# Kernel optimization log

Hardware: AMD Instinct MI355X
Metric: run time of the kernel (lower is better)

## Reference

```python
import jax, jax.numpy as jnp
import numpy as np
from jax import lax

N_QUBITS = 8
N_BLOCKS = 5

_H = jnp.array([[1.0, 1.0], [1.0, -1.0]], dtype=jnp.complex64) / np.sqrt(2.0).astype(np.float32)
# torchquantum PauliY.diagonalizing_gates = [Z, S, H] applied in order -> matrix H @ S @ Z = H @ diag(1, -1j)
_YROT = _H @ jnp.diag(jnp.array([1.0, -1j], dtype=jnp.complex64))


def apply_gate(st, U, wires):
    # st: [N, 2, 2, ..., 2] (n_qubits trailing axes); U: [2^k, 2^k]
    k = len(wires)
    axes = [w + 1 for w in wires]
    s = jnp.moveaxis(st, axes, list(range(1, k + 1)))
    shp = s.shape
    s = s.reshape(shp[0], 2 ** k, -1)
    s = jnp.einsum('ij,bjr->bir', U, s)
    return jnp.moveaxis(s.reshape(shp), list(range(1, k + 1)), axes)


def u3_mat(th, ph, lam):
    c = jnp.cos(0.5 * th).astype(jnp.complex64)
    s = jnp.sin(0.5 * th).astype(jnp.complex64)
    el = jnp.exp(1j * lam)
    ep = jnp.exp(1j * ph)
    return jnp.stack([jnp.stack([c, -el * s]), jnp.stack([ep * s, ep * el * c])])


def cu3_mat(th, ph, lam):
    M = jnp.eye(4, dtype=jnp.complex64)
    return M.at[2:, 2:].set(u3_mat(th, ph, lam))


def z_expvals(st):
    # <Z_w> for every wire from marginal probabilities
    n = st.ndim - 1
    mag = st.real ** 2 + st.imag ** 2
    outs = []
    for w in range(n):
        axes = tuple(a for a in range(1, n + 1) if a != w + 1)
        p = mag.sum(axes)  # [N, 2]
        outs.append(p[:, 0] - p[:, 1])
    return jnp.stack(outs, axis=1)


def quantum_conv(x, conv_w, conv_b, u3_params, cu3_params, fc_w, fc_b):
    n = N_QUBITS
    B, C, H, W = x.shape
    y = lax.conv_general_dilated(x, conv_w, (1, 1), 'SAME',
                                 dimension_numbers=('NCHW', 'OIHW', 'NCHW'))
    y = y + conv_b[None, :, None, None]
    ang = y.transpose(0, 2, 3, 1).reshape(-1, n)  # [B*H*W, n_qubits]
    Npx = ang.shape[0]
    # RY(theta)|0> encoding: product state of [cos(t/2), sin(t/2)] per wire
    c = jnp.cos(0.5 * ang)
    s = jnp.sin(0.5 * ang)
    st = jnp.stack([c[:, 0], s[:, 0]], axis=1).astype(jnp.complex64)
    for w in range(1, n):
        q = jnp.stack([c[:, w], s[:, w]], axis=1).astype(jnp.complex64)
        st = (st[:, :, None] * q[:, None, :]).reshape(Npx, -1)
    st = st.reshape((Npx,) + (2,) * n)
    # U3CU3Layer0: per block, U3 on each wire then circular CU3 ring
    for b in range(N_BLOCKS):
        for w in range(n):
            st = apply_gate(st, u3_mat(u3_params[b, w, 0], u3_params[b, w, 1], u3_params[b, w, 2]), [w])
        for w in range(n):
            st = apply_gate(st, cu3_mat(cu3_params[b, w, 0], cu3_params[b, w, 1], cu3_params[b, w, 2]), [w, (w + 1) % n])
    # MeasureAll(Z), then MeasureAll(X) and MeasureAll(Y) which MUTATE the device
    # state with their diagonalizing gates (torchquantum semantics)
    mz = z_expvals(st)
    for w in range(n):
        st = apply_gate(st, _H, [w])
    mx = z_expvals(st)
    for w in range(n):
        st = apply_gate(st, _YROT, [w])
    my = z_expvals(st)
    meas = jnp.concatenate([mz, mx, my], axis=1)  # [B*H*W, 3*n]
    out = meas @ fc_w.T + fc_b
    return out.reshape(B, H, W, -1).transpose(0, 3, 1, 2)


def setup_inputs() -> dict:
    key = jax.random.key(0)
    ks = jax.random.split(key, 7)
    n, cin, cout = N_QUBITS, 16, 32
    x = jax.random.normal(ks[0], (4, cin, 64, 64), dtype=jnp.float32)
    conv_w = jax.random.normal(ks[1], (n, cin, 3, 3), dtype=jnp.float32) / np.sqrt(cin * 9)
    conv_b = jax.random.normal(ks[2], (n,), dtype=jnp.float32) * 0.01
    u3_params = jax.random.uniform(ks[3], (N_BLOCKS, n, 3), dtype=jnp.float32, minval=-np.pi, maxval=np.pi)
    cu3_params = jax.random.uniform(ks[4], (N_BLOCKS, n, 3), dtype=jnp.float32, minval=-np.pi, maxval=np.pi)
    fc_w = jax.random.normal(ks[5], (cout, 3 * n), dtype=jnp.float32) / np.sqrt(3 * n)
    fc_b = jax.random.normal(ks[6], (cout,), dtype=jnp.float32) * 0.01
    return {'x': x, 'conv_w': conv_w, 'conv_b': conv_b, 'u3_params': u3_params,
            'cu3_params': cu3_params, 'fc_w': fc_w, 'fc_b': fc_b}


def reference(x, conv_w, conv_b, u3_params, cu3_params, fc_w, fc_b):
    return quantum_conv(x, conv_w, conv_b, u3_params, cu3_params, fc_w, fc_b)
```

## Files before the change

### kernel.cpp

```cpp
#include <hip/hip_runtime.h>

typedef float v2f __attribute__((ext_vector_type(2)));

template<int C>
__device__ __forceinline__ float dppmov(float x) {
  return __int_as_float(__builtin_amdgcn_update_dpp(0, __float_as_int(x), C, 0xF, 0xF, true));
}
__device__ __forceinline__ float bperm(float x, int a) {
  return __int_as_float(__builtin_amdgcn_ds_bpermute(a, __float_as_int(x)));
}
template<int M>
__device__ __forceinline__ float bfly(float x) {
  if constexpr (M == 1)      return dppmov<0xB1>(x);
  else if constexpr (M == 2) return dppmov<0x4E>(x);
  else if constexpr (M == 3) return dppmov<0x1B>(x);
  else if constexpr (M == 8) return dppmov<0x128>(x);
  else                       return dppmov<0x1B>(dppmov<0x141>(x));
}
template<int M>
__device__ __forceinline__ v2f bfly2(v2f v) {
  v2f o; o.x = bfly<M>(v.x); o.y = bfly<M>(v.y); return o;
}
__device__ __forceinline__ v2f sp(float s) { v2f v; v.x = s; v.y = s; return v; }
__device__ __forceinline__ v2f vfma(v2f a, v2f b, v2f c) {
  return __builtin_elementwise_fma(a, b, c);
}

template<int M, int CM>
__device__ __forceinline__ void crossG(v2f Sr[16], v2f Si[16],
    const float* g, int lane) {
  const bool hi = (lane & M) != 0;
  const bool ct = (lane & CM) != 0;
  float f0r = hi ? g[6]  : g[0],  f0i = hi ? g[7]  : g[1];
  float g0r = hi ? g[4]  : g[2],  g0i = hi ? g[5]  : g[3];
  float f1r = hi ? g[14] : g[8],  f1i = hi ? g[15] : g[9];
  float g1r = hi ? g[12] : g[10], g1i = hi ? g[13] : g[11];
  float fr = ct ? f1r : f0r, fi = ct ? f1i : f0i;
  float gr = ct ? g1r : g0r, gi = ct ? g1i : g0i;
  v2f vfr = sp(fr), vfi = sp(fi), vgr = sp(gr), vgi = sp(gi);
  v2f vfiN = sp(-fi), vgiN = sp(-gi);
#pragma unroll
  for (int r = 0; r < 16; ++r) {
    v2f pR = bfly2<M>(Sr[r]);
    v2f pI = bfly2<M>(Si[r]);
    v2f nR = vfma(vgiN, pI, vfma(vgr, pR, vfma(vfiN, Si[r], vfr * Sr[r])));
    v2f nI = vfma(vgi,  pR, vfma(vgr, pI, vfma(vfi,  Sr[r], vfr * Si[r])));
    Sr[r] = nR; Si[r] = nI;
  }
}

__device__ __forceinline__ void mixP(v2f& x0r, v2f& x0i, v2f& x1r, v2f& x1i,
    float m0r, float m0i, float m1r, float m1i,
    float m2r, float m2i, float m3r, float m3i) {
  v2f n0r = vfma(sp(-m1i), x1i, vfma(sp(m1r), x1r, vfma(sp(-m0i), x0i, sp(m0r) * x0r)));
  v2f n0i = vfma(sp( m1i), x1r, vfma(sp(m1r), x1i, vfma(sp( m0i), x0r, sp(m0r) * x0i)));
  v2f n1r = vfma(sp(-m3i), x1i, vfma(sp(m3r), x1r, vfma(sp(-m2i), x0i, sp(m2r) * x0r)));
  v2f n1i = vfma(sp( m3i), x1r, vfma(sp(m3r), x1i, vfma(sp( m2i), x0r, sp(m2r) * x0i)));
  x0r = n0r; x0i = n0i; x1r = n1r; x1i = n1i;
}

__device__ __forceinline__ void f4N(v2f Sr[16], v2f Si[16],
    const float* g, int lane) {
  const bool ct = (lane & 1) != 0;
  float m[8];
#pragma unroll
  for (int jj = 0; jj < 8; ++jj) m[jj] = ct ? g[8 + jj] : g[jj];
#pragma unroll
  for (int r = 0; r < 8; ++r)
    mixP(Sr[r], Si[r], Sr[r + 8], Si[r + 8],
         m[0], m[1], m[2], m[3], m[4], m[5], m[6], m[7]);
}
__device__ __forceinline__ void f5N(v2f Sr[16], v2f Si[16], const float* g) {
#pragma unroll
  for (int r = 0; r < 4; ++r)
    mixP(Sr[r], Si[r], Sr[r + 4], Si[r + 4],
         g[0], g[1], g[2], g[3], g[4], g[5], g[6], g[7]);
#pragma unroll
  for (int r = 8; r < 12; ++r)
    mixP(Sr[r], Si[r], Sr[r + 4], Si[r + 4],
         g[8], g[9], g[10], g[11], g[12], g[13], g[14], g[15]);
}
__device__ __forceinline__ void f67N(v2f Sr[16], v2f Si[16], const float* T) {
#pragma unroll
  for (int qd = 0; qd < 4; ++qd) {
    const int B = qd * 4;
    const float* M = T + (qd & 1) * 32;
    v2f ar0 = Sr[B+0], ai0 = Si[B+0], ar1 = Sr[B+1], ai1 = Si[B+1];
    v2f ar2 = Sr[B+2], ai2 = Si[B+2], ar3 = Sr[B+3], ai3 = Si[B+3];
#pragma unroll
    for (int rp = 0; rp < 4; ++rp) {
      const float* Mr = M + rp * 8;
      v2f nR = sp(Mr[0]) * ar0;
      nR = vfma(sp(-Mr[1]), ai0, nR);
      nR = vfma(sp( Mr[2]), ar1, nR);
      nR = vfma(sp(-Mr[3]), ai1, nR);
      nR = vfma(sp( Mr[4]), ar2, nR);
      nR = vfma(sp(-Mr[5]), ai2, nR);
      nR = vfma(sp( Mr[6]), ar3, nR);
      nR = vfma(sp(-Mr[7]), ai3, nR);
      v2f nI = sp(Mr[1]) * ar0;
      nI = vfma(sp(Mr[0]), ai0, nI);
      nI = vfma(sp(Mr[3]), ar1, nI);
      nI = vfma(sp(Mr[2]), ai1, nI);
      nI = vfma(sp(Mr[5]), ar2, nI);
      nI = vfma(sp(Mr[4]), ai2, nI);
      nI = vfma(sp(Mr[7]), ar3, nI);
      nI = vfma(sp(Mr[6]), ai3, nI);
      Sr[B + rp] = nR; Si[B + rp] = nI;
    }
  }
}
__device__ __forceinline__ void f8pN(v2f Sr[16], v2f Si[16],
    const float* g, int lane) {
  const bool hi = (lane & 8) != 0;
  float fr[2], fi[2], gr[2], gi[2];
  fr[0] = hi ? g[6]  : g[0];  fi[0] = hi ? g[7]  : g[1];
  gr[0] = hi ? g[4]  : g[2];  gi[0] = hi ? g[5]  : g[3];
  fr[1] = hi ? g[14] : g[8];  fi[1] = hi ? g[15] : g[9];
  gr[1] = hi ? g[12] : g[10]; gi[1] = hi ? g[13] : g[11];
#pragma unroll
  for (int r = 0; r < 16; ++r) {
    const int m = r & 1;
    v2f pR = bfly2<8>(Sr[r]);
    v2f pI = bfly2<8>(Si[r]);
    v2f nR = vfma(sp(-gi[m]), pI, vfma(sp(gr[m]), pR, vfma(sp(-fi[m]), Si[r], sp(fr[m]) * Sr[r])));
    v2f nI = vfma(sp( gi[m]), pR, vfma(sp(gr[m]), pI, vfma(sp( fi[m]), Sr[r], sp(fr[m]) * Si[r])));
    Sr[r] = nR; Si[r] = nI;
  }
}
__device__ __forceinline__ void f8N(v2f Sr[16], v2f Si[16],
    const float* g, int lane) {
  const bool hi = (lane & 8) != 0;
  const float fr = hi ? g[6] : g[0], fi = hi ? g[7] : g[1];
  const float gr = hi ? g[4] : g[2], gi = hi ? g[5] : g[3];
#pragma unroll
  for (int r = 1; r < 16; r += 2) {
    v2f pR = bfly2<8>(Sr[r]);
    v2f pI = bfly2<8>(Si[r]);
    v2f nR = vfma(sp(-gi), pI, vfma(sp(gr), pR, vfma(sp(-fi), Si[r], sp(fr) * Sr[r])));
    v2f nI = vfma(sp( gi), pR, vfma(sp(gr), pI, vfma(sp( fi), Sr[r], sp(fr) * Si[r])));
    Sr[r] = nR; Si[r] = nI;
  }
}

template<int M>
__device__ __forceinline__ void crossO(const v2f Sr[16], const v2f Si[16],
                                       v2f& re, v2f& im) {
  v2f r = sp(0.0f), i = sp(0.0f);
#pragma unroll
  for (int k = 0; k < 16; ++k) {
    v2f pr = bfly2<M>(Sr[k]);
    v2f pi = bfly2<M>(Si[k]);
    r = vfma(Sr[k], pr, r);
    r = vfma(Si[k], pi, r);
    i = vfma(Si[k], pr, i);
    i = vfma(-Sr[k], pi, i);
  }
  re = r; im = i;
}

__device__ __forceinline__ void mm2(const float* A, const float* B, float* D) {
  D[0] = A[0]*B[0] - A[1]*B[1] + A[2]*B[4] - A[3]*B[5];
  D[1] = A[0]*B[1] + A[1]*B[0] + A[2]*B[5] + A[3]*B[4];
  D[2] = A[0]*B[2] - A[1]*B[3] + A[2]*B[6] - A[3]*B[7];
  D[3] = A[0]*B[3] + A[1]*B[2] + A[2]*B[7] + A[3]*B[6];
  D[4] = A[4]*B[0] - A[5]*B[1] + A[6]*B[4] - A[7]*B[5];
  D[5] = A[4]*B[1] + A[5]*B[0] + A[6]*B[5] + A[7]*B[4];
  D[6] = A[4]*B[2] - A[5]*B[3] + A[6]*B[6] - A[7]*B[7];
  D[7] = A[4]*B[3] + A[5]*B[2] + A[6]*B[7] + A[7]*B[6];
}
__device__ __forceinline__ void u3fill(const float* src, float* o) {
  float th = src[0], ph = src[1], lam = src[2];
  float c = cosf(0.5f * th), s = sinf(0.5f * th);
  float cl = cosf(lam), sl = sinf(lam);
  float cp = cosf(ph), spv = sinf(ph);
  float cpl = cosf(ph + lam), spl = sinf(ph + lam);
  o[0] = c;        o[1] = 0.0f;
  o[2] = -cl * s;  o[3] = -sl * s;
  o[4] = cp * s;   o[5] = spv * s;
  o[6] = cpl * c;  o[7] = spl * c;
}

__global__ __launch_bounds__(256) void qconv_kernel(
    const float* __restrict__ x, const float* __restrict__ cw,
    const float* __restrict__ cb, const float* __restrict__ u3p,
    const float* __restrict__ cu3p, const float* __restrict__ fcw,
    const float* __restrict__ fcb, float* __restrict__ out) {
  __shared__ float Us[40][8];
  __shared__ float Cs[40][8];
  __shared__ float Gs[640];
  __shared__ float FCWs[32 * 29];
  __shared__ float F67t[320];

  {
    const int t = threadIdx.x;
    if (t < 40) u3fill(u3p + t * 3, Us[t]);
    if (t >= 64 && t < 104) u3fill(cu3p + (t - 64) * 3, Cs[t - 64]);
    for (int i = t; i < 32 * 29; i += 256) {
      int ch = i / 29, u = i - ch * 29;
      float v = 0.0f;
      if (u < 24) {
        float sc = (u >= 8 && (u & 7) >= 4) ? 2.0f : 1.0f;
        v = fcw[ch * 24 + u] * sc;
      }
      FCWs[i] = v;
    }
    __syncthreads();
    if (t == 0) {
#pragma unroll
      for (int j = 0; j < 8; ++j) Gs[j] = Us[0][j];
    } else if (t < 36) {
      int j = t - 1, b = j / 7, k = j % 7;
      float* dst = Gs + 8 + b * 112 + k * 16;
      const float* U = Us[b * 8 + k + 1];
      const float* C = Cs[b * 8 + k];
#pragma unroll
      for (int u = 0; u < 8; ++u) dst[u] = U[u];
      mm2(C, U, dst + 8);
    } else if (t < 40) {
      int b = t - 36;
      float* dst = Gs + 568 + b * 16;
      const float* U = Us[(b + 1) * 8];
      const float* C = Cs[b * 8 + 7];
#pragma unroll
      for (int u = 0; u < 8; ++u) dst[u] = U[u];
      mm2(U, C, dst + 8);
    } else if (t == 40) {
#pragma unroll
      for (int j = 0; j < 8; ++j) Gs[632 + j] = Cs[39][j];
    }
    __syncthreads();
    if (t >= 64 && t < 104) {
      int u = t - 64;
      int b = u >> 3, idx = u & 7;
      int ct = idx >> 2, rp = idx & 3;
      const float* M6 = Gs + 8 + b * 112 + 80 + ct * 8;
      int b1p = rp >> 1, b0p = rp & 1;
      const float* M7 = Gs + 8 + b * 112 + 96 + b1p * 8;
      float* dst = F67t + b * 64 + ct * 32 + rp * 8;
#pragma unroll
      for (int c = 0; c < 4; ++c) {
        int b1 = c >> 1, b0 = c & 1;
        float a_r = M6[(b1p * 2 + b1) * 2], a_i = M6[(b1p * 2 + b1) * 2 + 1];
        float b_r = M7[(b0p * 2 + b0) * 2], b_i = M7[(b0p * 2 + b0) * 2 + 1];
        dst[c * 2]     = a_r * b_r - a_i * b_i;
        dst[c * 2 + 1] = a_r * b_i + a_i * b_r;
      }
    }
    __syncthreads();
  }

  const int lane = threadIdx.x & 63;
  const int wid = __builtin_amdgcn_readfirstlane(
      (int)((blockIdx.x * blockDim.x + threadIdx.x) >> 6));
  const int p0 = wid * 8;
  const int q = lane & 15;

  float ang;
  {
    const int px = lane >> 3;
    const int oc = lane & 7;
    const int p  = p0 + px;
    const int b  = p >> 12;
    const int hh = (p >> 6) & 63;
    const int wim = p & 63;
    float acc = cb[oc];
#pragma unroll 4
    for (int ic = 0; ic < 16; ++ic) {
      const float* wp = cw + (oc * 16 + ic) * 9;
      const float* xp = x + (b * 16 + ic) * 4096;
#pragma unroll
      for (int kh = 0; kh < 3; ++kh) {
        int ih = hh + kh - 1;
        bool rok = (unsigned)ih < 64u;
        int ihc = rok ? ih : 0;
#pragma unroll
        for (int kw = 0; kw < 3; ++kw) {
          int iw = wim + kw - 1;
          bool ok = rok && ((unsigned)iw < 64u);
          int iwc = ((unsigned)iw < 64u) ? iw : 0;
          float xv = xp[ihc * 64 + iwc];
          acc = fmaf(ok ? xv : 0.0f, wp[kh * 3 + kw], acc);
        }
      }
    }
    ang = acc;
  }

  v2f Sr[16], Si[16];
  {
    const int gb = (lane & 48) << 2;
    float aA[8], aB[8];
#pragma unroll
    for (int w = 0; w < 8; ++w) {
      aA[w] = bperm(ang, gb + (w << 2));
      aB[w] = bperm(ang, gb + ((8 + w) << 2));
    }
    float cA[8], sA[8], cB[8], sB[8];
#pragma unroll
    for (int w = 0; w < 8; ++w) {
      __sincosf(0.5f * aA[w], &sA[w], &cA[w]);
      __sincosf(0.5f * aB[w], &sB[w], &cB[w]);
    }
    v2f c0; c0.x = cA[0]; c0.y = cB[0];
    v2f s0; s0.x = sA[0]; s0.y = sB[0];
    v2f c0r = vfma(sp(Gs[2]), s0, sp(Gs[0]) * c0);
    v2f c0i = vfma(sp(Gs[3]), s0, sp(Gs[1]) * c0);
    v2f s0r = vfma(sp(Gs[6]), s0, sp(Gs[4]) * c0);
    v2f s0i = vfma(sp(Gs[7]), s0, sp(Gs[5]) * c0);
    const bool w0 = (q & 8) != 0;
    v2f selR = w0 ? s0r : c0r;
    v2f selI = w0 ? s0i : c0i;
    float fA = ((q & 4) ? sA[1] : cA[1]) * ((q & 2) ? sA[2] : cA[2])
             * ((q & 1) ? sA[3] : cA[3]);
    float fB = ((q & 4) ? sB[1] : cB[1]) * ((q & 2) ? sB[2] : cB[2])
             * ((q & 1) ? sB[3] : cB[3]);
    v2f uu[4], vv[4];
    uu[0].x = cA[6]*cA[7]; uu[1].x = cA[6]*sA[7];
    uu[2].x = sA[6]*cA[7]; uu[3].x = sA[6]*sA[7];
    uu[0].y = cB[6]*cB[7]; uu[1].y = cB[6]*sB[7];
    uu[2].y = sB[6]*cB[7]; uu[3].y = sB[6]*sB[7];
    float vA0 = fA * cA[4], vA1 = fA * sA[4];
    float vB0 = fB * cB[4], vB1 = fB * sB[4];
    vv[0].x = vA0*cA[5]; vv[1].x = vA0*sA[5];
    vv[2].x = vA1*cA[5]; vv[3].x = vA1*sA[5];
    vv[0].y = vB0*cB[5]; vv[1].y = vB0*sB[5];
    vv[2].y = vB1*cB[5]; vv[3].y = vB1*sB[5];
#pragma unroll
    for (int r = 0; r < 16; ++r) {
      v2f base = vv[r >> 2] * uu[r & 3];
      Sr[r] = selR * base;
      Si[r] = selI * base;
    }
  }

  for (int b = 0; b < 5; ++b) {
    const float* base = Gs + 8 + b * 112;
    crossG<4, 8>(Sr, Si, base + 0, lane);
    crossG<2, 4>(Sr, Si, base + 16, lane);
    crossG<1, 2>(Sr, Si, base + 32, lane);
    f4N(Sr, Si, base + 48, lane);
    f5N(Sr, Si, base + 64);
    f67N(Sr, Si, F67t + b * 64);
    if (b < 4) f8pN(Sr, Si, Gs + 568 + b * 16, lane);
  }
  f8N(Sr, Si, Gs + 632, lane);

  float sg[4];
  sg[0] = (q & 8) ? -1.0f : 1.0f;
  sg[1] = (q & 4) ? -1.0f : 1.0f;
  sg[2] = (q & 2) ? -1.0f : 1.0f;
  sg[3] = (q & 1) ? -1.0f : 1.0f;

  v2f PT[24];
  {
    v2f re0, im0, re1, im1, re2, im2, re3, im3;
    crossO<8>(Sr, Si, re0, im0);
    crossO<4>(Sr, Si, re1, im1);
    crossO<2>(Sr, Si, re2, im2);
    crossO<1>(Sr, Si, re3, im3);
    PT[8]  = re0; PT[9]  = re1; PT[10] = re2; PT[11] = re3;
    PT[16] = sp(sg[0]) * im0; PT[17] = sp(sg[1]) * im1;
    PT[18] = sp(sg[2]) * im2; PT[19] = sp(sg[3]) * im3;

    v2f P[16];
#pragma unroll
    for (int r = 0; r < 16; ++r) P[r] = vfma(Si[r], Si[r], Sr[r] * Sr[r]);
    v2f t01[8];
#pragma unroll
    for (int k = 0; k < 8; ++k) t01[k] = P[2*k] + P[2*k+1];
    v2f q0 = t01[0] + t01[1], q1 = t01[2] + t01[3];
    v2f q2 = t01[4] + t01[5], q3 = t01[6] + t01[7];
    v2f h0 = q0 + q1, h1 = q2 + q3;
    v2f p  = h0 + h1;
    PT[4] = h0 - h1;
    PT[5] = (q0 - q1) + (q2 - q3);
    PT[6] = (t01[0]-t01[1]) + (t01[2]-t01[3])
          + (t01[4]-t01[5]) + (t01[6]-t01[7]);
    PT[7] = (P[0]-P[1]) + (P[2]-P[3]) + (P[4]-P[5]) + (P[6]-P[7])
          + (P[8]-P[9]) + (P[10]-P[11]) + (P[12]-P[13]) + (P[14]-P[15]);
    PT[0] = sp(sg[0]) * p; PT[1] = sp(sg[1]) * p;
    PT[2] = sp(sg[2]) * p; PT[3] = sp(sg[3]) * p;

    v2f re, im;
    re = sp(0.0f); im = sp(0.0f);
#pragma unroll
    for (int r = 0; r < 8; ++r) {
      re = vfma(Sr[r], Sr[r+8], re); re = vfma(Si[r], Si[r+8], re);
      im = vfma(Si[r], Sr[r+8], im); im = vfma(-Sr[r], Si[r+8], im);
    }
    PT[12] = re; PT[20] = im;
    re = sp(0.0f); im = sp(0.0f);
#pragma unroll
    for (int t = 0; t < 8; ++t) {
      const int lo = (t & 3) + (t >> 2) * 8;
      re = vfma(Sr[lo], Sr[lo+4], re); re = vfma(Si[lo], Si[lo+4], re);
      im = vfma(Si[lo], Sr[lo+4], im); im = vfma(-Sr[lo], Si[lo+4], im);
    }
    PT[13] = re; PT[21] = im;
    re = sp(0.0f); im = sp(0.0f);
#pragma unroll
    for (int t = 0; t < 8; ++t) {
      const int lo = (t & 1) + (t >> 1) * 4;
      re = vfma(Sr[lo], Sr[lo+2], re); re = vfma(Si[lo], Si[lo+2], re);
      im = vfma(Si[lo], Sr[lo+2], im); im = vfma(-Sr[lo], Si[lo+2], im);
    }
    PT[14] = re; PT[22] = im;
    re = sp(0.0f); im = sp(0.0f);
#pragma unroll
    for (int t = 0; t < 8; ++t) {
      const int lo = 2 * t;
      re = vfma(Sr[lo], Sr[lo+1], re); re = vfma(Si[lo], Si[lo+1], re);
      im = vfma(Si[lo], Sr[lo+1], im); im = vfma(-Sr[lo], Si[lo+1], im);
    }
    PT[15] = re; PT[23] = im;
  }

  const int j = q & 7;
  const bool isB = (q & 8) != 0;
  float mm[24];
#pragma unroll
  for (int t = 0; t < 24; ++t) {
    v2f v = PT[t] + bfly2<8>(PT[t]);
    float s = isB ? v.y : v.x;
    s += bfly<1>(s);
    s += bfly<2>(s);
    s += bfly<4>(s);
    mm[t] = s;
  }

  const int g = lane >> 4;
  const int p = p0 + 2 * g + (isB ? 1 : 0);
  const int ob = (p >> 12) * 131072 + (p & 4095);
#pragma unroll
  for (int k = 0; k < 4; ++k) {
    const int ch = 4 * j + k;
    const float* wr = FCWs + ch * 29;
    float acc = fcb[ch];
#pragma unroll
    for (int u = 0; u < 24; ++u) acc = fmaf(mm[u], wr[u], acc);
    out[ob + ch * 4096] = acc;
  }
}

extern "C" void kernel_launch(void* const* d_in, const int* in_sizes, int n_in,
                              void* d_out, int out_size, void* d_ws, size_t ws_size,
                              hipStream_t stream) {
  const float* x      = (const float*)d_in[0];
  const float* conv_w = (const float*)d_in[1];
  const float* conv_b = (const float*)d_in[2];
  const float* u3p    = (const float*)d_in[3];
  const float* cu3p   = (const float*)d_in[4];
  const float* fcw    = (const float*)d_in[5];
  const float* fcb    = (const float*)d_in[6];
  float* out = (float*)d_out;

  qconv_kernel<<<512, 256, 0, stream>>>(x, conv_w, conv_b, u3p, cu3p,
                                        fcw, fcb, out);
}
```

Baseline: 108.1 us.

## Prefetch gate coefficients from LDS into registers ahead of each gate stage

The gate-application loop now loads each stage's coefficients from shared memory into register arrays with 128-bit vector loads, one stage ahead of use. This is meant to hide LDS latency behind the butterfly arithmetic. It also switches the U3 trig setup to fast __sincosf and adds a min-blocks-per-CU launch bound of 2. The extra register arrays (about 96 floats) and the occupancy hint may raise register pressure or cause spills.

```diff
diff --git a/kernel.cpp b/kernel.cpp
--- a/kernel.cpp
+++ b/kernel.cpp
@@ -1,6 +1,7 @@
 #include <hip/hip_runtime.h>
 
 typedef float v2f __attribute__((ext_vector_type(2)));
+typedef float v4f __attribute__((ext_vector_type(4)));
 
 template<int C>
 __device__ __forceinline__ float dppmov(float x) {
@@ -24,6 +25,25 @@
 __device__ __forceinline__ v2f sp(float s) { v2f v; v.x = s; v.y = s; return v; }
 __device__ __forceinline__ v2f vfma(v2f a, v2f b, v2f c) {
   return __builtin_elementwise_fma(a, b, c);
+}
+
+__device__ __forceinline__ void ld16(float* d, const float* s) {
+  const v4f* p = (const v4f*)s;
+  v4f a = p[0], b = p[1], c = p[2], e = p[3];
+  d[0]=a.x; d[1]=a.y; d[2]=a.z; d[3]=a.w;
+  d[4]=b.x; d[5]=b.y; d[6]=b.z; d[7]=b.w;
+  d[8]=c.x; d[9]=c.y; d[10]=c.z; d[11]=c.w;
+  d[12]=e.x; d[13]=e.y; d[14]=e.z; d[15]=e.w;
+}
+__device__ __forceinline__ void ld8(float* d, const float* s) {
+  const v4f* p = (const v4f*)s;
+  v4f a = p[0], b = p[1];
+  d[0]=a.x; d[1]=a.y; d[2]=a.z; d[3]=a.w;
+  d[4]=b.x; d[5]=b.y; d[6]=b.z; d[7]=b.w;
+}
+__device__ __forceinline__ void ld64(float* d, const float* s) {
+#pragma unroll
+  for (int k = 0; k < 4; ++k) ld16(d + k * 16, s + k * 16);
 }
 
 template<int M, int CM>
@@ -171,26 +191,27 @@
 }
 __device__ __forceinline__ void u3fill(const float* src, float* o) {
   float th = src[0], ph = src[1], lam = src[2];
-  float c = cosf(0.5f * th), s = sinf(0.5f * th);
-  float cl = cosf(lam), sl = sinf(lam);
-  float cp = cosf(ph), spv = sinf(ph);
-  float cpl = cosf(ph + lam), spl = sinf(ph + lam);
+  float c, s, cl, sl, cp, spv, cpl, spl;
+  __sincosf(0.5f * th, &s, &c);
+  __sincosf(lam, &sl, &cl);
+  __sincosf(ph, &spv, &cp);
+  __sincosf(ph + lam, &spl, &cpl);
   o[0] = c;        o[1] = 0.0f;
   o[2] = -cl * s;  o[3] = -sl * s;
   o[4] = cp * s;   o[5] = spv * s;
   o[6] = cpl * c;  o[7] = spl * c;
 }
 
-__global__ __launch_bounds__(256) void qconv_kernel(
+__global__ __launch_bounds__(256, 2) void qconv_kernel(
     const float* __restrict__ x, const float* __restrict__ cw,
     const float* __restrict__ cb, const float* __restrict__ u3p,
     const float* __restrict__ cu3p, const float* __restrict__ fcw,
     const float* __restrict__ fcb, float* __restrict__ out) {
   __shared__ float Us[40][8];
   __shared__ float Cs[40][8];
-  __shared__ float Gs[640];
+  __shared__ __attribute__((aligned(16))) float Gs[640];
   __shared__ float FCWs[32 * 29];
-  __shared__ float F67t[320];
+  __shared__ __attribute__((aligned(16))) float F67t[320];
 
   {
     const int t = threadIdx.x;
@@ -334,17 +355,31 @@
     }
   }
 
-  for (int b = 0; b < 5; ++b) {
-    const float* base = Gs + 8 + b * 112;
-    crossG<4, 8>(Sr, Si, base + 0, lane);
-    crossG<2, 4>(Sr, Si, base + 16, lane);
-    crossG<1, 2>(Sr, Si, base + 32, lane);
-    f4N(Sr, Si, base + 48, lane);
-    f5N(Sr, Si, base + 64);
-    f67N(Sr, Si, F67t + b * 64);
-    if (b < 4) f8pN(Sr, Si, Gs + 568 + b * 16, lane);
-  }
-  f8N(Sr, Si, Gs + 632, lane);
+  {
+    float c0[16], c1[16], T[64];
+    ld16(c0, Gs + 8);
+    for (int b = 0; b < 5; ++b) {
+      const float* base = Gs + 8 + b * 112;
+      ld16(c1, base + 16);
+      crossG<4, 8>(Sr, Si, c0, lane);
+      ld16(c0, base + 32);
+      crossG<2, 4>(Sr, Si, c1, lane);
+      ld16(c1, base + 48);
+      crossG<1, 2>(Sr, Si, c0, lane);
+      ld16(c0, base + 64);
+      f4N(Sr, Si, c1, lane);
+      ld64(T, F67t + b * 64);
+      f5N(Sr, Si, c0);
+      if (b < 4) ld16(c1, Gs + 568 + b * 16);
+      else       ld8 (c1, Gs + 632);
+      f67N(Sr, Si, T);
+      if (b < 4) {
+        f8pN(Sr, Si, c1, lane);
+        ld16(c0, base + 112);
+      }
+    }
+    f8N(Sr, Si, c1, lane);
+  }
 
   float sg[4];
   sg[0] = (q & 8) ? -1.0f : 1.0f;
```

After: 110.4 us. 2.2% more time.
